# Performance work log

Measured on AMD Instinct MI355X. Metric: run time of the kernel, lower is better.

## Reference

```python
import jax, jax.numpy as jnp
import numpy as np

B, S, I, W, H = 32, 2048, 32, 20, 128  # batch, seq_len, input_size, window_size, hidden_size
LN_EPS = 1e-5


def setup_inputs() -> dict:
    key = jax.random.key(0)
    ks = jax.random.split(key, 12)
    sc = lambda fan: 1.0 / np.sqrt(fan)
    x = jax.random.normal(ks[0], (B, S, I), jnp.float32)
    # encoder: Linear(W*I -> H) + LayerNorm(H) (+ GELU, dropout inactive at eval)
    W_enc = jax.random.normal(ks[1], (W * I, H), jnp.float32) * sc(W * I)
    b_enc = jnp.zeros((H,), jnp.float32)
    gamma = jnp.ones((H,), jnp.float32)
    beta = jnp.zeros((H,), jnp.float32)
    # comparator: Linear(2H->H), GELU, Linear(H->H//2), GELU, Linear(H//2->1), Sigmoid
    W1 = jax.random.normal(ks[2], (2 * H, H), jnp.float32) * sc(2 * H)
    b1 = jnp.zeros((H,), jnp.float32)
    W2 = jax.random.normal(ks[3], (H, H // 2), jnp.float32) * sc(H)
    b2 = jnp.zeros((H // 2,), jnp.float32)
    W3 = jax.random.normal(ks[4], (H // 2, 1), jnp.float32) * sc(H // 2)
    b3 = jnp.zeros((1,), jnp.float32)
    return dict(x=x, W_enc=W_enc, b_enc=b_enc, gamma=gamma, beta=beta,
                W1=W1, b1=b1, W2=W2, b2=b2, W3=W3, b3=b3)


def _gelu(v):
    return jax.nn.gelu(v, approximate=False)  # torch nn.GELU default is exact erf


def reference(x, W_enc, b_enc, gamma, beta, W1, b1, W2, b2, W3, b3):
    Bs, Ss, Is = x.shape
    Wd = W_enc.shape[0] // Is  # window_size
    nwin = Ss - Wd + 1
    # gather all sliding windows once: (B, nwin, Wd*I)
    idx = jnp.arange(nwin)[:, None] + jnp.arange(Wd)[None, :]
    win = x[:, idx, :].reshape(Bs, nwin, Wd * Is)
    # encoder: one big GEMM over all windows (before(t) == window at t-Wd, after(t) == window at t)
    h = win @ W_enc + b_enc
    mu = jnp.mean(h, axis=-1, keepdims=True)
    var = jnp.mean((h - mu) ** 2, axis=-1, keepdims=True)
    enc = _gelu((h - mu) / jnp.sqrt(var + LN_EPS) * gamma + beta)  # (B, nwin, H)
    T = Ss - 2 * Wd  # number of valid changepoint positions t in [Wd, Ss-Wd)
    combined = jnp.concatenate([enc[:, :T], enc[:, Wd:Wd + T]], axis=-1)  # (B, T, 2H)
    z = _gelu(combined @ W1 + b1)
    z = _gelu(z @ W2 + b2)
    p = jax.nn.sigmoid((z @ W3 + b3)[..., 0])  # (B, T)
    probs = jnp.pad(p, ((0, 0), (Wd, Wd)))  # zero pad to (B, S)
    return probs, probs > 0.5
```

## Files before the change

### kernel.cpp

```cpp
#include <hip/hip_runtime.h>
#include <hip/hip_bf16.h>
#include <math.h>

namespace {

constexpr int kB = 32;
constexpr int kS = 2048;
constexpr int kI = 32;
constexpr int kW = 20;
constexpr int kH = 128;
constexpr int kNwin = kS - kW + 1;
constexpr int kT = kS - 2 * kW;
constexpr float kEps = 1e-5f;
constexpr int FCAP = 4096;
constexpr float kMargin = 1e-3f;

typedef __attribute__((ext_vector_type(8))) short short8;
typedef __attribute__((ext_vector_type(8))) unsigned short ush8;
typedef __attribute__((ext_vector_type(4))) float f32x4;

__device__ __forceinline__ unsigned short f2bf(float f) {
    unsigned u = __builtin_bit_cast(unsigned, f);
    u += 0x7FFFu + ((u >> 16) & 1u);
    return (unsigned short)(u >> 16);
}
__device__ __forceinline__ float bf2f(unsigned short h) {
    unsigned u = ((unsigned)h) << 16;
    return __builtin_bit_cast(float, u);
}
__device__ __forceinline__ void split2(float v, unsigned short& hi, unsigned short& lo) {
    hi = f2bf(v);
    lo = f2bf(v - bf2f(hi));
}
__device__ __forceinline__ float gelu_exact(float v) {
    return 0.5f * v * (1.0f + erff(v * 0.70710678118654752440f));
}

constexpr size_t ENCP_OFF = 0;
constexpr size_t WETH_OFF = 33554432;
constexpr size_t WETL_OFF = WETH_OFF + 163840;
constexpr size_t W1TH_OFF = WETL_OFF + 163840;
constexpr size_t W1TL_OFF = W1TH_OFF + 65536;
constexpr size_t W2TH_OFF = W1TL_OFF + 65536;
constexpr size_t W2TL_OFF = W2TH_OFF + 16384;
constexpr size_t FC_OFF   = W2TL_OFF + 16384;
constexpr size_t FL_OFF   = FC_OFF + 64;

__global__ void prep_kernel(const float* __restrict__ Wenc, const float* __restrict__ W1,
                            const float* __restrict__ W2,
                            unsigned short* __restrict__ WeTh, unsigned short* __restrict__ WeTl,
                            unsigned short* __restrict__ W1Th, unsigned short* __restrict__ W1Tl,
                            unsigned short* __restrict__ W2Th, unsigned short* __restrict__ W2Tl)
{
    const int tid = blockIdx.x * blockDim.x + threadIdx.x;
    const int nth = gridDim.x * blockDim.x;
    for (int i = tid; i < kH * 640; i += nth) {
        int n = i / 640, k = i - n * 640;
        split2(Wenc[(size_t)k * kH + n], WeTh[i], WeTl[i]);
    }
    for (int i = tid; i < kH * 256; i += nth) {
        int n = i >> 8, k = i & 255;
        split2(W1[(size_t)k * kH + n], W1Th[i], W1Tl[i]);
    }
    for (int i = tid; i < 64 * kH; i += nth) {
        int n = i >> 7, k = i & 127;
        split2(W2[(size_t)k * 64 + n], W2Th[i], W2Tl[i]);
    }
}

constexpr int AP = 40;

__global__ __launch_bounds__(256, 2)
void enc_kernel(const float* __restrict__ x,
                const unsigned short* __restrict__ WeTh, const unsigned short* __restrict__ WeTl,
                const float* __restrict__ benc, const float* __restrict__ gma,
                const float* __restrict__ bta, unsigned* __restrict__ encp)
{
    __shared__ unsigned short xsh[148 * AP];
    __shared__ unsigned short xsl[148 * AP];
    __shared__ unsigned short wth[128 * AP];
    __shared__ unsigned short wtl[128 * AP];
    __shared__ float prm[384];

    const int tid = threadIdx.x, b = blockIdx.y, t0 = blockIdx.x * 128;
    const int l = tid & 63, w = tid >> 6;
    const int cb = l & 15, rg = l >> 4;

    if (tid < 128) { prm[tid] = benc[tid]; prm[128 + tid] = gma[tid]; prm[256 + tid] = bta[tid]; }

    const float4* x4 = reinterpret_cast<const float4*>(x + (size_t)b * kS * kI);
    for (int i = tid; i < 148 * 8; i += 256) {
        int r = i >> 3, q = i & 7;
        int gr = t0 + r; if (gr > kS - 1) gr = kS - 1;
        float4 v = x4[gr * 8 + q];
        unsigned short h0, h1, h2, h3, l0, l1, l2, l3;
        split2(v.x, h0, l0); split2(v.y, h1, l1); split2(v.z, h2, l2); split2(v.w, h3, l3);
        *reinterpret_cast<uint2*>(&xsh[r * AP + q * 4]) =
            make_uint2((unsigned)h0 | ((unsigned)h1 << 16), (unsigned)h2 | ((unsigned)h3 << 16));
        *reinterpret_cast<uint2*>(&xsl[r * AP + q * 4]) =
            make_uint2((unsigned)l0 | ((unsigned)l1 << 16), (unsigned)l2 | ((unsigned)l3 << 16));
    }

    f32x4 acc[2][8];
    #pragma unroll
    for (int mi = 0; mi < 2; ++mi)
        #pragma unroll
        for (int nf = 0; nf < 8; ++nf) acc[mi][nf] = f32x4{0.f, 0.f, 0.f, 0.f};

    for (int kc = 0; kc < 20; ++kc) {
        __syncthreads();
        #pragma unroll
        for (int u = 0; u < 2; ++u) {
            int i = tid + 256 * u;
            int n = i >> 2, q = i & 3;
            *reinterpret_cast<ush8*>(&wth[n * AP + q * 8]) =
                *reinterpret_cast<const ush8*>(WeTh + (size_t)n * 640 + kc * 32 + q * 8);
            *reinterpret_cast<ush8*>(&wtl[n * AP + q * 8]) =
                *reinterpret_cast<const ush8*>(WeTl + (size_t)n * 640 + kc * 32 + q * 8);
        }
        __syncthreads();
        const int a0o = (w * 32 + cb + kc) * AP + rg * 8;
        const int a1o = a0o + 16 * AP;
        short8 a0h = *reinterpret_cast<const short8*>(&xsh[a0o]);
        short8 a0l = *reinterpret_cast<const short8*>(&xsl[a0o]);
        short8 a1h = *reinterpret_cast<const short8*>(&xsh[a1o]);
        short8 a1l = *reinterpret_cast<const short8*>(&xsl[a1o]);
        #pragma unroll
        for (int nf = 0; nf < 8; ++nf) {
            const int bo = (nf * 16 + cb) * AP + rg * 8;
            short8 bh = *reinterpret_cast<const short8*>(&wth[bo]);
            short8 bl = *reinterpret_cast<const short8*>(&wtl[bo]);
            acc[0][nf] = __builtin_amdgcn_mfma_f32_16x16x32_bf16(a0h, bh, acc[0][nf], 0, 0, 0);
            acc[0][nf] = __builtin_amdgcn_mfma_f32_16x16x32_bf16(a0l, bh, acc[0][nf], 0, 0, 0);
            acc[0][nf] = __builtin_amdgcn_mfma_f32_16x16x32_bf16(a0h, bl, acc[0][nf], 0, 0, 0);
            acc[1][nf] = __builtin_amdgcn_mfma_f32_16x16x32_bf16(a1h, bh, acc[1][nf], 0, 0, 0);
            acc[1][nf] = __builtin_amdgcn_mfma_f32_16x16x32_bf16(a1l, bh, acc[1][nf], 0, 0, 0);
            acc[1][nf] = __builtin_amdgcn_mfma_f32_16x16x32_bf16(a1h, bl, acc[1][nf], 0, 0, 0);
        }
    }

    #pragma unroll
    for (int mi = 0; mi < 2; ++mi) {
        #pragma unroll
        for (int r = 0; r < 4; ++r) {
            const int rl = w * 32 + mi * 16 + rg * 4 + r;
            const int t = t0 + rl;
            float h[8];
            float s = 0.f;
            #pragma unroll
            for (int nf = 0; nf < 8; ++nf) { h[nf] = acc[mi][nf][r] + prm[nf * 16 + cb]; s += h[nf]; }
            s += __shfl_xor(s, 1); s += __shfl_xor(s, 2); s += __shfl_xor(s, 4); s += __shfl_xor(s, 8);
            const float mu = s * (1.f / 128.f);
            float s2 = 0.f;
            #pragma unroll
            for (int nf = 0; nf < 8; ++nf) { h[nf] -= mu; s2 += h[nf] * h[nf]; }
            s2 += __shfl_xor(s2, 1); s2 += __shfl_xor(s2, 2); s2 += __shfl_xor(s2, 4); s2 += __shfl_xor(s2, 8);
            const float rstd = 1.f / sqrtf(s2 * (1.f / 128.f) + kEps);
            if (t < kNwin) {
                unsigned* dst = encp + ((size_t)(b * kS + t)) * kH;
                #pragma unroll
                for (int nf = 0; nf < 8; ++nf) {
                    float v = gelu_exact(h[nf] * rstd * prm[128 + nf * 16 + cb] + prm[256 + nf * 16 + cb]);
                    unsigned short hi, lo;
                    split2(v, hi, lo);
                    dst[nf * 16 + cb] = (unsigned)hi | ((unsigned)lo << 16);
                }
            }
        }
    }
}

__global__ __launch_bounds__(256, 2)
void cmp_kernel(const unsigned* __restrict__ encp,
                const unsigned short* __restrict__ W1Th, const unsigned short* __restrict__ W1Tl,
                const float* __restrict__ b1,
                const unsigned short* __restrict__ W2Th, const unsigned short* __restrict__ W2Tl,
                const float* __restrict__ b2, const float* __restrict__ W3,
                const float* __restrict__ b3, float* __restrict__ out,
                int* __restrict__ fcnt, unsigned* __restrict__ flist)
{
    __shared__ __align__(16) unsigned short pool[27648];
    __shared__ float prm[192];

    unsigned short* esh = pool;
    unsigned short* esl = pool + 2560;
    unsigned short* z1h = pool;
    unsigned short* z1l = pool + 8704;
    unsigned short* wth = pool + 17408;
    unsigned short* wtl = pool + 22528;
    float* z2f = reinterpret_cast<float*>(pool);

    const int tid = threadIdx.x, b = blockIdx.y, t0 = blockIdx.x * 64;
    const int l = tid & 63, w = tid >> 6;
    const int cb = l & 15, rg = l >> 4;

    if (tid < 128) prm[tid] = b1[tid];
    else if (tid < 192) prm[tid] = b2[tid - 128];

    f32x4 acc1[8];
    #pragma unroll
    for (int nf = 0; nf < 8; ++nf) acc1[nf] = f32x4{0.f, 0.f, 0.f, 0.f};

    for (int kc = 0; kc < 8; ++kc) {
        __syncthreads();
        const int ro = (kc < 4) ? 0 : kW, co = (kc & 3) * 32;
        {
            const int r = tid >> 2, q = tid & 3;
            int gr = t0 + ro + r; if (gr > kNwin - 1) gr = kNwin - 1;
            const unsigned* src = encp + ((size_t)(b * kS + gr)) * kH + co + q * 8;
            const uint4 v0 = *reinterpret_cast<const uint4*>(src);
            const uint4 v1 = *reinterpret_cast<const uint4*>(src + 4);
            *reinterpret_cast<uint2*>(&esh[r * AP + q * 8]) =
                make_uint2((v0.x & 0xFFFFu) | ((v0.y & 0xFFFFu) << 16),
                           (v0.z & 0xFFFFu) | ((v0.w & 0xFFFFu) << 16));
            *reinterpret_cast<uint2*>(&esh[r * AP + q * 8 + 4]) =
                make_uint2((v1.x & 0xFFFFu) | ((v1.y & 0xFFFFu) << 16),
                           (v1.z & 0xFFFFu) | ((v1.w & 0xFFFFu) << 16));
            *reinterpret_cast<uint2*>(&esl[r * AP + q * 8]) =
                make_uint2((v0.x >> 16) | (v0.y & 0xFFFF0000u),
                           (v0.z >> 16) | (v0.w & 0xFFFF0000u));
            *reinterpret_cast<uint2*>(&esl[r * AP + q * 8 + 4]) =
                make_uint2((v1.x >> 16) | (v1.y & 0xFFFF0000u),
                           (v1.z >> 16) | (v1.w & 0xFFFF0000u));
        }
        #pragma unroll
        for (int u = 0; u < 2; ++u) {
            int i = tid + 256 * u;
            int n = i >> 2, q = i & 3;
            *reinterpret_cast<ush8*>(&wth[n * AP + q * 8]) =
                *reinterpret_cast<const ush8*>(W1Th + (size_t)n * 256 + kc * 32 + q * 8);
            *reinterpret_cast<ush8*>(&wtl[n * AP + q * 8]) =
                *reinterpret_cast<const ush8*>(W1Tl + (size_t)n * 256 + kc * 32 + q * 8);
        }
        __syncthreads();
        const int ao = (w * 16 + cb) * AP + rg * 8;
        short8 ah = *reinterpret_cast<const short8*>(&esh[ao]);
        short8 al = *reinterpret_cast<const short8*>(&esl[ao]);
        #pragma unroll
        for (int nf = 0; nf < 8; ++nf) {
            const int bo = (nf * 16 + cb) * AP + rg * 8;
            short8 bh = *reinterpret_cast<const short8*>(&wth[bo]);
            short8 bl = *reinterpret_cast<const short8*>(&wtl[bo]);
            acc1[nf] = __builtin_amdgcn_mfma_f32_16x16x32_bf16(ah, bh, acc1[nf], 0, 0, 0);
            acc1[nf] = __builtin_amdgcn_mfma_f32_16x16x32_bf16(al, bh, acc1[nf], 0, 0, 0);
            acc1[nf] = __builtin_amdgcn_mfma_f32_16x16x32_bf16(ah, bl, acc1[nf], 0, 0, 0);
        }
    }
    __syncthreads();
    #pragma unroll
    for (int r = 0; r < 4; ++r) {
        const int row = w * 16 + rg * 4 + r;
        #pragma unroll
        for (int nf = 0; nf < 8; ++nf) {
            float v = gelu_exact(acc1[nf][r] + prm[nf * 16 + cb]);
            unsigned short hi, lo;
            split2(v, hi, lo);
            z1h[row * 136 + nf * 16 + cb] = hi;
            z1l[row * 136 + nf * 16 + cb] = lo;
        }
    }

    f32x4 acc2[4];
    #pragma unroll
    for (int nf = 0; nf < 4; ++nf) acc2[nf] = f32x4{0.f, 0.f, 0.f, 0.f};

    for (int kc = 0; kc < 4; ++kc) {
        __syncthreads();
        {
            int n = tid >> 2, q = tid & 3;
            *reinterpret_cast<ush8*>(&wth[n * AP + q * 8]) =
                *reinterpret_cast<const ush8*>(W2Th + (size_t)n * 128 + kc * 32 + q * 8);
            *reinterpret_cast<ush8*>(&wtl[n * AP + q * 8]) =
                *reinterpret_cast<const ush8*>(W2Tl + (size_t)n * 128 + kc * 32 + q * 8);
        }
        __syncthreads();
        const int ao = (w * 16 + cb) * 136 + kc * 32 + rg * 8;
        short8 ah = *reinterpret_cast<const short8*>(&z1h[ao]);
        short8 al = *reinterpret_cast<const short8*>(&z1l[ao]);
        #pragma unroll
        for (int nf = 0; nf < 4; ++nf) {
            const int bo = (nf * 16 + cb) * AP + rg * 8;
            short8 bh = *reinterpret_cast<const short8*>(&wth[bo]);
            short8 bl = *reinterpret_cast<const short8*>(&wtl[bo]);
            acc2[nf] = __builtin_amdgcn_mfma_f32_16x16x32_bf16(ah, bh, acc2[nf], 0, 0, 0);
            acc2[nf] = __builtin_amdgcn_mfma_f32_16x16x32_bf16(al, bh, acc2[nf], 0, 0, 0);
            acc2[nf] = __builtin_amdgcn_mfma_f32_16x16x32_bf16(ah, bl, acc2[nf], 0, 0, 0);
        }
    }
    __syncthreads();
    #pragma unroll
    for (int r = 0; r < 4; ++r) {
        const int row = w * 16 + rg * 4 + r;
        #pragma unroll
        for (int nf = 0; nf < 4; ++nf)
            z2f[row * 68 + nf * 16 + cb] = gelu_exact(acc2[nf][r] + prm[128 + nf * 16 + cb]);
    }
    __syncthreads();

    if (tid < 64) {
        const int t = t0 + tid;
        if (t < kT) {
            float s = 0.f;
            #pragma unroll 8
            for (int k = 0; k < 64; ++k) s = fmaf(z2f[tid * 68 + k], W3[k], s);
            const float p = 1.f / (1.f + expf(-(s + b3[0])));
            out[(size_t)b * kS + t + kW] = p;
            out[(size_t)kB * kS + (size_t)b * kS + t + kW] = (p > 0.5f) ? 1.f : 0.f;
            if (fabsf(p - 0.5f) < kMargin) {
                int idx = atomicAdd(fcnt, 1);
                if (idx < FCAP) flist[idx] = ((unsigned)b << 16) | (unsigned)t;
            }
        }
    }
}

__global__ __launch_bounds__(256, 4)
void fix2_kernel(const float* __restrict__ x, const float* __restrict__ Wenc,
                 const float* __restrict__ benc, const float* __restrict__ gma,
                 const float* __restrict__ bta, const float* __restrict__ W1,
                 const float* __restrict__ b1, const float* __restrict__ W2,
                 const float* __restrict__ b2, const float* __restrict__ W3,
                 const float* __restrict__ b3, const int* __restrict__ fcnt,
                 const unsigned* __restrict__ flist, float* __restrict__ out)
{
    __shared__ float xw[1280];
    __shared__ float es[256];
    __shared__ float z1s[128];
    __shared__ float z2s[64];
    __shared__ float wred[4];

    const int tid = threadIdx.x;
    int n = *fcnt; if (n > FCAP) n = FCAP;

    for (int i = blockIdx.x; i < n; i += gridDim.x) {
        const unsigned e = flist[i];
        const int b = (int)(e >> 16), t = (int)(e & 0xFFFF);
        __syncthreads();
        for (int j = tid; j < 320; j += 256) {
            int r = (j >= 160) ? 1 : 0, u = j - r * 160;
            const float4 v = *reinterpret_cast<const float4*>(
                x + ((size_t)b * kS + t + r * kW) * kI + u * 4);
            *reinterpret_cast<float4*>(&xw[r * 640 + u * 4]) = v;
        }
        __syncthreads();
        const int r = tid >> 7, c = tid & 127;
        float h = 0.f;
        const float* xr = &xw[r * 640];
        #pragma unroll 16
        for (int k = 0; k < 640; ++k) h = fmaf(xr[k], Wenc[(size_t)k * kH + c], h);
        h += benc[c];
        float s = h;
        #pragma unroll
        for (int m = 1; m < 64; m <<= 1) s += __shfl_xor(s, m, 64);
        if ((tid & 63) == 0) wred[tid >> 6] = s;
        __syncthreads();
        const float mu = (wred[r * 2] + wred[r * 2 + 1]) * (1.f / 128.f);
        const float d = h - mu;
        float s2 = d * d;
        #pragma unroll
        for (int m = 1; m < 64; m <<= 1) s2 += __shfl_xor(s2, m, 64);
        __syncthreads();
        if ((tid & 63) == 0) wred[tid >> 6] = s2;
        __syncthreads();
        const float var = (wred[r * 2] + wred[r * 2 + 1]) * (1.f / 128.f);
        es[tid] = gelu_exact(d * (1.f / sqrtf(var + kEps)) * gma[c] + bta[c]);
        __syncthreads();
        if (tid < kH) {
            float z = 0.f;
            #pragma unroll 16
            for (int k = 0; k < 256; ++k) z = fmaf(es[k], W1[(size_t)k * kH + tid], z);
            z1s[tid] = gelu_exact(z + b1[tid]);
        }
        __syncthreads();
        if (tid < 64) {
            float z = 0.f;
            #pragma unroll 16
            for (int k = 0; k < kH; ++k) z = fmaf(z1s[k], W2[(size_t)k * 64 + tid], z);
            z2s[tid] = gelu_exact(z + b2[tid]);
        }
        __syncthreads();
        if (tid < 64) {
            float s3 = z2s[tid] * W3[tid];
            #pragma unroll
            for (int m = 1; m < 64; m <<= 1) s3 += __shfl_xor(s3, m, 64);
            if (tid == 0) {
                const float p = 1.f / (1.f + expf(-(s3 + b3[0])));
                out[(size_t)b * kS + t + kW] = p;
                out[(size_t)kB * kS + (size_t)b * kS + t + kW] = (p > 0.5f) ? 1.f : 0.f;
            }
        }
        __syncthreads();
    }
}

}

extern "C" void kernel_launch(void* const* d_in, const int* in_sizes, int n_in,
                              void* d_out, int out_size, void* d_ws, size_t ws_size,
                              hipStream_t stream)
{
    const float* x    = (const float*)d_in[0];
    const float* Wenc = (const float*)d_in[1];
    const float* benc = (const float*)d_in[2];
    const float* gma  = (const float*)d_in[3];
    const float* bta  = (const float*)d_in[4];
    const float* W1   = (const float*)d_in[5];
    const float* b1   = (const float*)d_in[6];
    const float* W2   = (const float*)d_in[7];
    const float* b2   = (const float*)d_in[8];
    const float* W3   = (const float*)d_in[9];
    const float* b3   = (const float*)d_in[10];
    float* out = (float*)d_out;

    char* ws = (char*)d_ws;
    unsigned* encp        = (unsigned*)(ws + ENCP_OFF);
    unsigned short* WeTh  = (unsigned short*)(ws + WETH_OFF);
    unsigned short* WeTl  = (unsigned short*)(ws + WETL_OFF);
    unsigned short* W1Th  = (unsigned short*)(ws + W1TH_OFF);
    unsigned short* W1Tl  = (unsigned short*)(ws + W1TL_OFF);
    unsigned short* W2Th  = (unsigned short*)(ws + W2TH_OFF);
    unsigned short* W2Tl  = (unsigned short*)(ws + W2TL_OFF);
    int* fcnt             = (int*)(ws + FC_OFF);
    unsigned* flist       = (unsigned*)(ws + FL_OFF);

    hipMemsetAsync(d_out, 0, (size_t)out_size * sizeof(float), stream);
    hipMemsetAsync(fcnt, 0, 64, stream);

    prep_kernel<<<256, 256, 0, stream>>>(Wenc, W1, W2, WeTh, WeTl, W1Th, W1Tl, W2Th, W2Tl);
    enc_kernel<<<dim3(16, kB), 256, 0, stream>>>(x, WeTh, WeTl, benc, gma, bta, encp);
    cmp_kernel<<<dim3(32, kB), 256, 0, stream>>>(encp, W1Th, W1Tl, b1, W2Th, W2Tl, b2,
                                                 W3, b3, out, fcnt, flist);
    fix2_kernel<<<4096, 256, 0, stream>>>(x, Wenc, benc, gma, bta, W1, b1, W2, b2, W3, b3,
                                          fcnt, flist, out);
}
```

Before: 137.6 us.

## Double-buffer weight and activation tiles with register prefetch and swizzled LDS layout

The encoder and comparator GEMM loops now prefetch the next K-chunk of weights (and encoder activations) into registers while the MFMAs on the current chunk run, then write them to the other half of a double-buffered LDS area. This drops one barrier per iteration and hides global load latency behind compute. Weight tiles also move from a padded row stride to an XOR-swizzled 32-element layout to avoid LDS bank conflicts without padding. The cost is more registers held for the prefetch and a larger shared pool in the encoder, which could lower occupancy under the 2-blocks launch bound.

```diff
diff --git a/kernel.cpp b/kernel.cpp
--- a/kernel.cpp
+++ b/kernel.cpp
@@ -34,6 +34,9 @@
 }
 __device__ __forceinline__ float gelu_exact(float v) {
     return 0.5f * v * (1.0f + erff(v * 0.70710678118654752440f));
+}
+__device__ __forceinline__ int wsw(int n, int q) {
+    return n * 32 + ((q ^ ((n >> 1) & 3)) << 3);
 }
 
 constexpr size_t ENCP_OFF = 0;
@@ -76,11 +79,11 @@
                 const float* __restrict__ benc, const float* __restrict__ gma,
                 const float* __restrict__ bta, unsigned* __restrict__ encp)
 {
-    __shared__ unsigned short xsh[148 * AP];
-    __shared__ unsigned short xsl[148 * AP];
-    __shared__ unsigned short wth[128 * AP];
-    __shared__ unsigned short wtl[128 * AP];
+    __shared__ __align__(16) unsigned short pool[28144];
     __shared__ float prm[384];
+
+    unsigned short* xsh = pool;
+    unsigned short* xsl = pool + 5880;
 
     const int tid = threadIdx.x, b = blockIdx.y, t0 = blockIdx.x * 128;
     const int l = tid & 63, w = tid >> 6;
@@ -89,7 +92,7 @@
     if (tid < 128) { prm[tid] = benc[tid]; prm[128 + tid] = gma[tid]; prm[256 + tid] = bta[tid]; }
 
     const float4* x4 = reinterpret_cast<const float4*>(x + (size_t)b * kS * kI);
-    for (int i = tid; i < 148 * 8; i += 256) {
+    for (int i = tid; i < 147 * 8; i += 256) {
         int r = i >> 3, q = i & 7;
         int gr = t0 + r; if (gr > kS - 1) gr = kS - 1;
         float4 v = x4[gr * 8 + q];
@@ -101,35 +104,49 @@
             make_uint2((unsigned)l0 | ((unsigned)l1 << 16), (unsigned)l2 | ((unsigned)l3 << 16));
     }
 
+    const int n0 = tid >> 2, q0 = tid & 3;
+    const int wd0 = wsw(n0, q0), wd1 = wsw(n0 + 64, q0);
+    ush8 pwh0, pwl0, pwh1, pwl1;
+#define ELOADW(kc) { \
+    const unsigned short* sh = WeTh + (size_t)n0 * 640 + (kc) * 32 + q0 * 8; \
+    const unsigned short* sl = WeTl + (size_t)n0 * 640 + (kc) * 32 + q0 * 8; \
+    pwh0 = *reinterpret_cast<const ush8*>(sh); \
+    pwl0 = *reinterpret_cast<const ush8*>(sl); \
+    pwh1 = *reinterpret_cast<const ush8*>(sh + 64 * 640); \
+    pwl1 = *reinterpret_cast<const ush8*>(sl + 64 * 640); }
+#define EWRITEW(buf) { \
+    unsigned short* WH = pool + 11760 + (buf) * 8192; \
+    unsigned short* WL = WH + 4096; \
+    *reinterpret_cast<ush8*>(&WH[wd0]) = pwh0; \
+    *reinterpret_cast<ush8*>(&WH[wd1]) = pwh1; \
+    *reinterpret_cast<ush8*>(&WL[wd0]) = pwl0; \
+    *reinterpret_cast<ush8*>(&WL[wd1]) = pwl1; }
+
+    ELOADW(0); EWRITEW(0);
+    __syncthreads();
+
     f32x4 acc[2][8];
     #pragma unroll
     for (int mi = 0; mi < 2; ++mi)
         #pragma unroll
         for (int nf = 0; nf < 8; ++nf) acc[mi][nf] = f32x4{0.f, 0.f, 0.f, 0.f};
 
+    const int wb_r = cb * 32 + ((rg ^ ((cb >> 1) & 3)) << 3);
+
     for (int kc = 0; kc < 20; ++kc) {
-        __syncthreads();
-        #pragma unroll
-        for (int u = 0; u < 2; ++u) {
-            int i = tid + 256 * u;
-            int n = i >> 2, q = i & 3;
-            *reinterpret_cast<ush8*>(&wth[n * AP + q * 8]) =
-                *reinterpret_cast<const ush8*>(WeTh + (size_t)n * 640 + kc * 32 + q * 8);
-            *reinterpret_cast<ush8*>(&wtl[n * AP + q * 8]) =
-                *reinterpret_cast<const ush8*>(WeTl + (size_t)n * 640 + kc * 32 + q * 8);
-        }
-        __syncthreads();
+        const int cur = kc & 1;
+        if (kc < 19) ELOADW(kc + 1);
+        const unsigned short* WH = pool + 11760 + cur * 8192;
+        const unsigned short* WL = WH + 4096;
         const int a0o = (w * 32 + cb + kc) * AP + rg * 8;
-        const int a1o = a0o + 16 * AP;
         short8 a0h = *reinterpret_cast<const short8*>(&xsh[a0o]);
         short8 a0l = *reinterpret_cast<const short8*>(&xsl[a0o]);
-        short8 a1h = *reinterpret_cast<const short8*>(&xsh[a1o]);
-        short8 a1l = *reinterpret_cast<const short8*>(&xsl[a1o]);
+        short8 a1h = *reinterpret_cast<const short8*>(&xsh[a0o + 16 * AP]);
+        short8 a1l = *reinterpret_cast<const short8*>(&xsl[a0o + 16 * AP]);
         #pragma unroll
         for (int nf = 0; nf < 8; ++nf) {
-            const int bo = (nf * 16 + cb) * AP + rg * 8;
-            short8 bh = *reinterpret_cast<const short8*>(&wth[bo]);
-            short8 bl = *reinterpret_cast<const short8*>(&wtl[bo]);
+            short8 bh = *reinterpret_cast<const short8*>(&WH[nf * 512 + wb_r]);
+            short8 bl = *reinterpret_cast<const short8*>(&WL[nf * 512 + wb_r]);
             acc[0][nf] = __builtin_amdgcn_mfma_f32_16x16x32_bf16(a0h, bh, acc[0][nf], 0, 0, 0);
             acc[0][nf] = __builtin_amdgcn_mfma_f32_16x16x32_bf16(a0l, bh, acc[0][nf], 0, 0, 0);
             acc[0][nf] = __builtin_amdgcn_mfma_f32_16x16x32_bf16(a0h, bl, acc[0][nf], 0, 0, 0);
@@ -137,7 +154,11 @@
             acc[1][nf] = __builtin_amdgcn_mfma_f32_16x16x32_bf16(a1l, bh, acc[1][nf], 0, 0, 0);
             acc[1][nf] = __builtin_amdgcn_mfma_f32_16x16x32_bf16(a1h, bl, acc[1][nf], 0, 0, 0);
         }
-    }
+        if (kc < 19) EWRITEW(cur ^ 1);
+        __syncthreads();
+    }
+#undef ELOADW
+#undef EWRITEW
 
     #pragma unroll
     for (int mi = 0; mi < 2; ++mi) {
@@ -179,16 +200,8 @@
                 const float* __restrict__ b3, float* __restrict__ out,
                 int* __restrict__ fcnt, unsigned* __restrict__ flist)
 {
-    __shared__ __align__(16) unsigned short pool[27648];
+    __shared__ __align__(16) unsigned short pool[26624];
     __shared__ float prm[192];
-
-    unsigned short* esh = pool;
-    unsigned short* esl = pool + 2560;
-    unsigned short* z1h = pool;
-    unsigned short* z1l = pool + 8704;
-    unsigned short* wth = pool + 17408;
-    unsigned short* wtl = pool + 22528;
-    float* z2f = reinterpret_cast<float*>(pool);
 
     const int tid = threadIdx.x, b = blockIdx.y, t0 = blockIdx.x * 64;
     const int l = tid & 63, w = tid >> 6;
@@ -197,56 +210,95 @@
     if (tid < 128) prm[tid] = b1[tid];
     else if (tid < 192) prm[tid] = b2[tid - 128];
 
+    const int er = tid >> 2, eq = tid & 3;
+    const int n0 = tid >> 2, q0 = tid & 3;
+    const int wd0 = wsw(n0, q0), wd1 = wsw(n0 + 64, q0);
+    const int wb_r = cb * 32 + ((rg ^ ((cb >> 1) & 3)) << 3);
+
+    uint4 pe0, pe1;
+    ush8 p1h0, p1l0, p1h1, p1l1;
+#define CLOADES(kc) { \
+    const int ro = ((kc) < 4) ? 0 : kW, co = ((kc) & 3) * 32; \
+    int gr = t0 + ro + er; if (gr > kNwin - 1) gr = kNwin - 1; \
+    const unsigned* src = encp + ((size_t)(b * kS + gr)) * kH + co + eq * 8; \
+    pe0 = *reinterpret_cast<const uint4*>(src); \
+    pe1 = *reinterpret_cast<const uint4*>(src + 4); }
+#define CWRITEES(buf) { \
+    unsigned short* EH = pool + (buf) * 5120; \
+    unsigned short* EL = EH + 2560; \
+    *reinterpret_cast<uint2*>(&EH[er * AP + eq * 8]) = \
+        make_uint2((pe0.x & 0xFFFFu) | ((pe0.y & 0xFFFFu) << 16), \
+                   (pe0.z & 0xFFFFu) | ((pe0.w & 0xFFFFu) << 16)); \
+    *reinterpret_cast<uint2*>(&EH[er * AP + eq * 8 + 4]) = \
+        make_uint2((pe1.x & 0xFFFFu) | ((pe1.y & 0xFFFFu) << 16), \
+                   (pe1.z & 0xFFFFu) | ((pe1.w & 0xFFFFu) << 16)); \
+    *reinterpret_cast<uint2*>(&EL[er * AP + eq * 8]) = \
+        make_uint2((pe0.x >> 16) | (pe0.y & 0xFFFF0000u), \
+                   (pe0.z >> 16) | (pe0.w & 0xFFFF0000u)); \
+    *reinterpret_cast<uint2*>(&EL[er * AP + eq * 8 + 4]) = \
+        make_uint2((pe1.x >> 16) | (pe1.y & 0xFFFF0000u), \
+                   (pe1.z >> 16) | (pe1.w & 0xFFFF0000u)); }
+#define CLOADW1(kc) { \
+    const unsigned short* sh = W1Th + (size_t)n0 * 256 + (kc) * 32 + q0 * 8; \
+    const unsigned short* sl = W1Tl + (size_t)n0 * 256 + (kc) * 32 + q0 * 8; \
+    p1h0 = *reinterpret_cast<const ush8*>(sh); \
+    p1l0 = *reinterpret_cast<const ush8*>(sl); \
+    p1h1 = *reinterpret_cast<const ush8*>(sh + 64 * 256); \
+    p1l1 = *reinterpret_cast<const ush8*>(sl + 64 * 256); }
+#define CWRITEW1(buf) { \
+    unsigned short* WH = pool + 10240 + (buf) * 8192; \
+    unsigned short* WL = WH + 4096; \
+    *reinterpret_cast<ush8*>(&WH[wd0]) = p1h0; \
+    *reinterpret_cast<ush8*>(&WH[wd1]) = p1h1; \
+    *reinterpret_cast<ush8*>(&WL[wd0]) = p1l0; \
+    *reinterpret_cast<ush8*>(&WL[wd1]) = p1l1; }
+
+    CLOADES(0); CLOADW1(0); CWRITEES(0); CWRITEW1(0);
+    __syncthreads();
+
     f32x4 acc1[8];
     #pragma unroll
     for (int nf = 0; nf < 8; ++nf) acc1[nf] = f32x4{0.f, 0.f, 0.f, 0.f};
 
     for (int kc = 0; kc < 8; ++kc) {
-        __syncthreads();
-        const int ro = (kc < 4) ? 0 : kW, co = (kc & 3) * 32;
-        {
-            const int r = tid >> 2, q = tid & 3;
-            int gr = t0 + ro + r; if (gr > kNwin - 1) gr = kNwin - 1;
-            const unsigned* src = encp + ((size_t)(b * kS + gr)) * kH + co + q * 8;
-            const uint4 v0 = *reinterpret_cast<const uint4*>(src);
-            const uint4 v1 = *reinterpret_cast<const uint4*>(src + 4);
-            *reinterpret_cast<uint2*>(&esh[r * AP + q * 8]) =
-                make_uint2((v0.x & 0xFFFFu) | ((v0.y & 0xFFFFu) << 16),
-                           (v0.z & 0xFFFFu) | ((v0.w & 0xFFFFu) << 16));
-            *reinterpret_cast<uint2*>(&esh[r * AP + q * 8 + 4]) =
-                make_uint2((v1.x & 0xFFFFu) | ((v1.y & 0xFFFFu) << 16),
-                           (v1.z & 0xFFFFu) | ((v1.w & 0xFFFFu) << 16));
-            *reinterpret_cast<uint2*>(&esl[r * AP + q * 8]) =
-                make_uint2((v0.x >> 16) | (v0.y & 0xFFFF0000u),
-                           (v0.z >> 16) | (v0.w & 0xFFFF0000u));
-            *reinterpret_cast<uint2*>(&esl[r * AP + q * 8 + 4]) =
-                make_uint2((v1.x >> 16) | (v1.y & 0xFFFF0000u),
-                           (v1.z >> 16) | (v1.w & 0xFFFF0000u));
-        }
-        #pragma unroll
-        for (int u = 0; u < 2; ++u) {
-            int i = tid + 256 * u;
-            int n = i >> 2, q = i & 3;
-            *reinterpret_cast<ush8*>(&wth[n * AP + q * 8]) =
-                *reinterpret_cast<const ush8*>(W1Th + (size_t)n * 256 + kc * 32 + q * 8);
-            *reinterpret_cast<ush8*>(&wtl[n * AP + q * 8]) =
-                *reinterpret_cast<const ush8*>(W1Tl + (size_t)n * 256 + kc * 32 + q * 8);
-        }
-        __syncthreads();
+        const int cur = kc & 1;
+        if (kc < 7) { CLOADES(kc + 1); CLOADW1(kc + 1); }
+        const unsigned short* EH = pool + cur * 5120;
+        const unsigned short* EL = EH + 2560;
+        const unsigned short* WH = pool + 10240 + cur * 8192;
+        const unsigned short* WL = WH + 4096;
         const int ao = (w * 16 + cb) * AP + rg * 8;
-        short8 ah = *reinterpret_cast<const short8*>(&esh[ao]);
-        short8 al = *reinterpret_cast<const short8*>(&esl[ao]);
+        short8 ah = *reinterpret_cast<const short8*>(&EH[ao]);
+        short8 al = *reinterpret_cast<const short8*>(&EL[ao]);
         #pragma unroll
         for (int nf = 0; nf < 8; ++nf) {
-            const int bo = (nf * 16 + cb) * AP + rg * 8;
-            short8 bh = *reinterpret_cast<const short8*>(&wth[bo]);
-            short8 bl = *reinterpret_cast<const short8*>(&wtl[bo]);
+            short8 bh = *reinterpret_cast<const short8*>(&WH[nf * 512 + wb_r]);
+            short8 bl = *reinterpret_cast<const short8*>(&WL[nf * 512 + wb_r]);
             acc1[nf] = __builtin_amdgcn_mfma_f32_16x16x32_bf16(ah, bh, acc1[nf], 0, 0, 0);
             acc1[nf] = __builtin_amdgcn_mfma_f32_16x16x32_bf16(al, bh, acc1[nf], 0, 0, 0);
             acc1[nf] = __builtin_amdgcn_mfma_f32_16x16x32_bf16(ah, bl, acc1[nf], 0, 0, 0);
         }
-    }
-    __syncthreads();
+        if (kc < 7) { CWRITEES(cur ^ 1); CWRITEW1(cur ^ 1); }
+        __syncthreads();
+    }
+#undef CLOADES
+#undef CWRITEES
+#undef CLOADW1
+#undef CWRITEW1
+
+    unsigned short* z1h = pool;
+    unsigned short* z1l = pool + 8704;
+    ush8 p2h, p2l;
+#define CLOADW2(kc) { \
+    p2h = *reinterpret_cast<const ush8*>(W2Th + (size_t)n0 * 128 + (kc) * 32 + q0 * 8); \
+    p2l = *reinterpret_cast<const ush8*>(W2Tl + (size_t)n0 * 128 + (kc) * 32 + q0 * 8); }
+#define CWRITEW2(buf) { \
+    unsigned short* WH = pool + 17408 + (buf) * 4096; \
+    unsigned short* WL = WH + 2048; \
+    *reinterpret_cast<ush8*>(&WH[wd0]) = p2h; \
+    *reinterpret_cast<ush8*>(&WL[wd0]) = p2l; }
+
+    CLOADW2(0);
     #pragma unroll
     for (int r = 0; r < 4; ++r) {
         const int row = w * 16 + rg * 4 + r;
@@ -259,35 +311,36 @@
             z1l[row * 136 + nf * 16 + cb] = lo;
         }
     }
+    CWRITEW2(0);
+    __syncthreads();
 
     f32x4 acc2[4];
     #pragma unroll
     for (int nf = 0; nf < 4; ++nf) acc2[nf] = f32x4{0.f, 0.f, 0.f, 0.f};
 
     for (int kc = 0; kc < 4; ++kc) {
-        __syncthreads();
-        {
-            int n = tid >> 2, q = tid & 3;
-            *reinterpret_cast<ush8*>(&wth[n * AP + q * 8]) =
-                *reinterpret_cast<const ush8*>(W2Th + (size_t)n * 128 + kc * 32 + q * 8);
-            *reinterpret_cast<ush8*>(&wtl[n * AP + q * 8]) =
-                *reinterpret_cast<const ush8*>(W2Tl + (size_t)n * 128 + kc * 32 + q * 8);
-        }
-        __syncthreads();
+        const int cur = kc & 1;
+        if (kc < 3) CLOADW2(kc + 1);
+        const unsigned short* WH = pool + 17408 + cur * 4096;
+        const unsigned short* WL = WH + 2048;
         const int ao = (w * 16 + cb) * 136 + kc * 32 + rg * 8;
         short8 ah = *reinterpret_cast<const short8*>(&z1h[ao]);
         short8 al = *reinterpret_cast<const short8*>(&z1l[ao]);
         #pragma unroll
         for (int nf = 0; nf < 4; ++nf) {
-            const int bo = (nf * 16 + cb) * AP + rg * 8;
-            short8 bh = *reinterpret_cast<const short8*>(&wth[bo]);
-            short8 bl = *reinterpret_cast<const short8*>(&wtl[bo]);
+            short8 bh = *reinterpret_cast<const short8*>(&WH[nf * 512 + wb_r]);
+            short8 bl = *reinterpret_cast<const short8*>(&WL[nf * 512 + wb_r]);
             acc2[nf] = __builtin_amdgcn_mfma_f32_16x16x32_bf16(ah, bh, acc2[nf], 0, 0, 0);
             acc2[nf] = __builtin_amdgcn_mfma_f32_16x16x32_bf16(al, bh, acc2[nf], 0, 0, 0);
             acc2[nf] = __builtin_amdgcn_mfma_f32_16x16x32_bf16(ah, bl, acc2[nf], 0, 0, 0);
         }
-    }
-    __syncthreads();
+        if (kc < 3) CWRITEW2(cur ^ 1);
+        __syncthreads();
+    }
+#undef CLOADW2
+#undef CWRITEW2
+
+    float* z2f = reinterpret_cast<float*>(pool);
     #pragma unroll
     for (int r = 0; r < 4; ++r) {
         const int row = w * 16 + rg * 4 + r;
```

Result: no change. 136.7 us (-0.6%).

## Enlarge encoder tile to 256 rows and stage cmp encodings once in LDS

Applied to the files above, without the earlier changes.

The encoder kernel now processes 256 windows per block with 512 threads, so each staged weight chunk serves twice as many rows and the x halo overhead is amortised. LN parameters move from shared memory into registers. The comparator kernel loads the full 84-row encoding slab into LDS once, up front, instead of re-reading global memory per K chunk, and unpacks the hi/lo bf16 halves at fragment-load time. Shared memory per cmp block rises to about 64KB, which may reduce occupancy.

```diff
diff --git a/kernel.cpp b/kernel.cpp
--- a/kernel.cpp
+++ b/kernel.cpp
@@ -69,27 +69,25 @@
 }
 
 constexpr int AP = 40;
-
-__global__ __launch_bounds__(256, 2)
+constexpr int EXR = 275;
+
+__global__ __launch_bounds__(512, 2)
 void enc_kernel(const float* __restrict__ x,
                 const unsigned short* __restrict__ WeTh, const unsigned short* __restrict__ WeTl,
                 const float* __restrict__ benc, const float* __restrict__ gma,
                 const float* __restrict__ bta, unsigned* __restrict__ encp)
 {
-    __shared__ unsigned short xsh[148 * AP];
-    __shared__ unsigned short xsl[148 * AP];
+    __shared__ unsigned short xsh[EXR * AP];
+    __shared__ unsigned short xsl[EXR * AP];
     __shared__ unsigned short wth[128 * AP];
     __shared__ unsigned short wtl[128 * AP];
-    __shared__ float prm[384];
-
-    const int tid = threadIdx.x, b = blockIdx.y, t0 = blockIdx.x * 128;
+
+    const int tid = threadIdx.x, b = blockIdx.y, t0 = blockIdx.x * 256;
     const int l = tid & 63, w = tid >> 6;
     const int cb = l & 15, rg = l >> 4;
 
-    if (tid < 128) { prm[tid] = benc[tid]; prm[128 + tid] = gma[tid]; prm[256 + tid] = bta[tid]; }
-
     const float4* x4 = reinterpret_cast<const float4*>(x + (size_t)b * kS * kI);
-    for (int i = tid; i < 148 * 8; i += 256) {
+    for (int i = tid; i < EXR * 8; i += 512) {
         int r = i >> 3, q = i & 7;
         int gr = t0 + r; if (gr > kS - 1) gr = kS - 1;
         float4 v = x4[gr * 8 + q];
@@ -109,22 +107,20 @@
 
     for (int kc = 0; kc < 20; ++kc) {
         __syncthreads();
-        #pragma unroll
-        for (int u = 0; u < 2; ++u) {
-            int i = tid + 256 * u;
-            int n = i >> 2, q = i & 3;
+        {
+            const int n = tid >> 2, q = tid & 3;
+            const size_t so = (size_t)n * 640 + kc * 32 + q * 8;
             *reinterpret_cast<ush8*>(&wth[n * AP + q * 8]) =
-                *reinterpret_cast<const ush8*>(WeTh + (size_t)n * 640 + kc * 32 + q * 8);
+                *reinterpret_cast<const ush8*>(WeTh + so);
             *reinterpret_cast<ush8*>(&wtl[n * AP + q * 8]) =
-                *reinterpret_cast<const ush8*>(WeTl + (size_t)n * 640 + kc * 32 + q * 8);
+                *reinterpret_cast<const ush8*>(WeTl + so);
         }
         __syncthreads();
         const int a0o = (w * 32 + cb + kc) * AP + rg * 8;
-        const int a1o = a0o + 16 * AP;
         short8 a0h = *reinterpret_cast<const short8*>(&xsh[a0o]);
         short8 a0l = *reinterpret_cast<const short8*>(&xsl[a0o]);
-        short8 a1h = *reinterpret_cast<const short8*>(&xsh[a1o]);
-        short8 a1l = *reinterpret_cast<const short8*>(&xsl[a1o]);
+        short8 a1h = *reinterpret_cast<const short8*>(&xsh[a0o + 16 * AP]);
+        short8 a1l = *reinterpret_cast<const short8*>(&xsl[a0o + 16 * AP]);
         #pragma unroll
         for (int nf = 0; nf < 8; ++nf) {
             const int bo = (nf * 16 + cb) * AP + rg * 8;
@@ -139,6 +135,13 @@
         }
     }
 
+    float bv[8], gv[8], btv[8];
+    #pragma unroll
+    for (int nf = 0; nf < 8; ++nf) {
+        bv[nf]  = benc[nf * 16 + cb];
+        gv[nf]  = gma[nf * 16 + cb];
+        btv[nf] = bta[nf * 16 + cb];
+    }
     #pragma unroll
     for (int mi = 0; mi < 2; ++mi) {
         #pragma unroll
@@ -148,7 +151,7 @@
             float h[8];
             float s = 0.f;
             #pragma unroll
-            for (int nf = 0; nf < 8; ++nf) { h[nf] = acc[mi][nf][r] + prm[nf * 16 + cb]; s += h[nf]; }
+            for (int nf = 0; nf < 8; ++nf) { h[nf] = acc[mi][nf][r] + bv[nf]; s += h[nf]; }
             s += __shfl_xor(s, 1); s += __shfl_xor(s, 2); s += __shfl_xor(s, 4); s += __shfl_xor(s, 8);
             const float mu = s * (1.f / 128.f);
             float s2 = 0.f;
@@ -160,7 +163,7 @@
                 unsigned* dst = encp + ((size_t)(b * kS + t)) * kH;
                 #pragma unroll
                 for (int nf = 0; nf < 8; ++nf) {
-                    float v = gelu_exact(h[nf] * rstd * prm[128 + nf * 16 + cb] + prm[256 + nf * 16 + cb]);
+                    float v = gelu_exact(h[nf] * rstd * gv[nf] + btv[nf]);
                     unsigned short hi, lo;
                     split2(v, hi, lo);
                     dst[nf * 16 + cb] = (unsigned)hi | ((unsigned)lo << 16);
@@ -169,6 +172,8 @@
         }
     }
 }
+
+constexpr int ESP = 132;
 
 __global__ __launch_bounds__(256, 2)
 void cmp_kernel(const unsigned* __restrict__ encp,
@@ -179,23 +184,23 @@
                 const float* __restrict__ b3, float* __restrict__ out,
                 int* __restrict__ fcnt, unsigned* __restrict__ flist)
 {
-    __shared__ __align__(16) unsigned short pool[27648];
-    __shared__ float prm[192];
-
-    unsigned short* esh = pool;
-    unsigned short* esl = pool + 2560;
-    unsigned short* z1h = pool;
-    unsigned short* z1l = pool + 8704;
-    unsigned short* wth = pool + 17408;
-    unsigned short* wtl = pool + 22528;
-    float* z2f = reinterpret_cast<float*>(pool);
+    __shared__ __align__(16) unsigned char poolb[64832];
+
+    unsigned* es         = reinterpret_cast<unsigned*>(poolb);
+    unsigned short* wt1h = reinterpret_cast<unsigned short*>(poolb + 44352);
+    unsigned short* wt1l = reinterpret_cast<unsigned short*>(poolb + 54592);
 
     const int tid = threadIdx.x, b = blockIdx.y, t0 = blockIdx.x * 64;
     const int l = tid & 63, w = tid >> 6;
     const int cb = l & 15, rg = l >> 4;
 
-    if (tid < 128) prm[tid] = b1[tid];
-    else if (tid < 192) prm[tid] = b2[tid - 128];
+    for (int i = tid; i < 84 * 32; i += 256) {
+        int r = i >> 5, u = i & 31;
+        int gr = t0 + r; if (gr > kNwin - 1) gr = kNwin - 1;
+        const uint4 v = *reinterpret_cast<const uint4*>(
+            encp + ((size_t)(b * kS + gr)) * kH + u * 4);
+        *reinterpret_cast<uint4*>(&es[r * ESP + u * 4]) = v;
+    }
 
     f32x4 acc1[8];
     #pragma unroll
@@ -203,56 +208,50 @@
 
     for (int kc = 0; kc < 8; ++kc) {
         __syncthreads();
-        const int ro = (kc < 4) ? 0 : kW, co = (kc & 3) * 32;
-        {
-            const int r = tid >> 2, q = tid & 3;
-            int gr = t0 + ro + r; if (gr > kNwin - 1) gr = kNwin - 1;
-            const unsigned* src = encp + ((size_t)(b * kS + gr)) * kH + co + q * 8;
-            const uint4 v0 = *reinterpret_cast<const uint4*>(src);
-            const uint4 v1 = *reinterpret_cast<const uint4*>(src + 4);
-            *reinterpret_cast<uint2*>(&esh[r * AP + q * 8]) =
-                make_uint2((v0.x & 0xFFFFu) | ((v0.y & 0xFFFFu) << 16),
-                           (v0.z & 0xFFFFu) | ((v0.w & 0xFFFFu) << 16));
-            *reinterpret_cast<uint2*>(&esh[r * AP + q * 8 + 4]) =
-                make_uint2((v1.x & 0xFFFFu) | ((v1.y & 0xFFFFu) << 16),
-                           (v1.z & 0xFFFFu) | ((v1.w & 0xFFFFu) << 16));
-            *reinterpret_cast<uint2*>(&esl[r * AP + q * 8]) =
-                make_uint2((v0.x >> 16) | (v0.y & 0xFFFF0000u),
-                           (v0.z >> 16) | (v0.w & 0xFFFF0000u));
-            *reinterpret_cast<uint2*>(&esl[r * AP + q * 8 + 4]) =
-                make_uint2((v1.x >> 16) | (v1.y & 0xFFFF0000u),
-                           (v1.z >> 16) | (v1.w & 0xFFFF0000u));
-        }
         #pragma unroll
         for (int u = 0; u < 2; ++u) {
             int i = tid + 256 * u;
             int n = i >> 2, q = i & 3;
-            *reinterpret_cast<ush8*>(&wth[n * AP + q * 8]) =
-                *reinterpret_cast<const ush8*>(W1Th + (size_t)n * 256 + kc * 32 + q * 8);
-            *reinterpret_cast<ush8*>(&wtl[n * AP + q * 8]) =
-                *reinterpret_cast<const ush8*>(W1Tl + (size_t)n * 256 + kc * 32 + q * 8);
-        }
-        __syncthreads();
-        const int ao = (w * 16 + cb) * AP + rg * 8;
-        short8 ah = *reinterpret_cast<const short8*>(&esh[ao]);
-        short8 al = *reinterpret_cast<const short8*>(&esl[ao]);
+            const size_t so = (size_t)n * 256 + kc * 32 + q * 8;
+            *reinterpret_cast<ush8*>(&wt1h[n * AP + q * 8]) =
+                *reinterpret_cast<const ush8*>(W1Th + so);
+            *reinterpret_cast<ush8*>(&wt1l[n * AP + q * 8]) =
+                *reinterpret_cast<const ush8*>(W1Tl + so);
+        }
+        __syncthreads();
+        const int ro = (kc < 4) ? 0 : kW, co = (kc & 3) * 32;
+        const unsigned* ep = es + (w * 16 + cb + ro) * ESP + co + rg * 8;
+        const uint4 v0 = *reinterpret_cast<const uint4*>(ep);
+        const uint4 v1 = *reinterpret_cast<const uint4*>(ep + 4);
+        const uint4 ahw = make_uint4(
+            (v0.x & 0xFFFFu) | ((v0.y & 0xFFFFu) << 16), (v0.z & 0xFFFFu) | ((v0.w & 0xFFFFu) << 16),
+            (v1.x & 0xFFFFu) | ((v1.y & 0xFFFFu) << 16), (v1.z & 0xFFFFu) | ((v1.w & 0xFFFFu) << 16));
+        const uint4 alw = make_uint4(
+            (v0.x >> 16) | (v0.y & 0xFFFF0000u), (v0.z >> 16) | (v0.w & 0xFFFF0000u),
+            (v1.x >> 16) | (v1.y & 0xFFFF0000u), (v1.z >> 16) | (v1.w & 0xFFFF0000u));
+        short8 ah = __builtin_bit_cast(short8, ahw);
+        short8 al = __builtin_bit_cast(short8, alw);
         #pragma unroll
         for (int nf = 0; nf < 8; ++nf) {
             const int bo = (nf * 16 + cb) * AP + rg * 8;
-            short8 bh = *reinterpret_cast<const short8*>(&wth[bo]);
-            short8 bl = *reinterpret_cast<const short8*>(&wtl[bo]);
+            short8 bh = *reinterpret_cast<const short8*>(&wt1h[bo]);
+            short8 bl = *reinterpret_cast<const short8*>(&wt1l[bo]);
             acc1[nf] = __builtin_amdgcn_mfma_f32_16x16x32_bf16(ah, bh, acc1[nf], 0, 0, 0);
             acc1[nf] = __builtin_amdgcn_mfma_f32_16x16x32_bf16(al, bh, acc1[nf], 0, 0, 0);
             acc1[nf] = __builtin_amdgcn_mfma_f32_16x16x32_bf16(ah, bl, acc1[nf], 0, 0, 0);
         }
     }
     __syncthreads();
+    unsigned short* z1h = reinterpret_cast<unsigned short*>(poolb);
+    unsigned short* z1l = reinterpret_cast<unsigned short*>(poolb + 17408);
+    unsigned short* w2h = reinterpret_cast<unsigned short*>(poolb + 34816);
+    unsigned short* w2l = reinterpret_cast<unsigned short*>(poolb + 39936);
     #pragma unroll
     for (int r = 0; r < 4; ++r) {
         const int row = w * 16 + rg * 4 + r;
         #pragma unroll
         for (int nf = 0; nf < 8; ++nf) {
-            float v = gelu_exact(acc1[nf][r] + prm[nf * 16 + cb]);
+            float v = gelu_exact(acc1[nf][r] + b1[nf * 16 + cb]);
             unsigned short hi, lo;
             split2(v, hi, lo);
             z1h[row * 136 + nf * 16 + cb] = hi;
@@ -267,11 +266,12 @@
     for (int kc = 0; kc < 4; ++kc) {
         __syncthreads();
         {
-            int n = tid >> 2, q = tid & 3;
-            *reinterpret_cast<ush8*>(&wth[n * AP + q * 8]) =
-                *reinterpret_cast<const ush8*>(W2Th + (size_t)n * 128 + kc * 32 + q * 8);
-            *reinterpret_cast<ush8*>(&wtl[n * AP + q * 8]) =
-                *reinterpret_cast<const ush8*>(W2Tl + (size_t)n * 128 + kc * 32 + q * 8);
+            const int n = tid >> 2, q = tid & 3;
+            const size_t so = (size_t)n * 128 + kc * 32 + q * 8;
+            *reinterpret_cast<ush8*>(&w2h[n * AP + q * 8]) =
+                *reinterpret_cast<const ush8*>(W2Th + so);
+            *reinterpret_cast<ush8*>(&w2l[n * AP + q * 8]) =
+                *reinterpret_cast<const ush8*>(W2Tl + so);
         }
         __syncthreads();
         const int ao = (w * 16 + cb) * 136 + kc * 32 + rg * 8;
@@ -280,20 +280,21 @@
         #pragma unroll
         for (int nf = 0; nf < 4; ++nf) {
             const int bo = (nf * 16 + cb) * AP + rg * 8;
-            short8 bh = *reinterpret_cast<const short8*>(&wth[bo]);
-            short8 bl = *reinterpret_cast<const short8*>(&wtl[bo]);
+            short8 bh = *reinterpret_cast<const short8*>(&w2h[bo]);
+            short8 bl = *reinterpret_cast<const short8*>(&w2l[bo]);
             acc2[nf] = __builtin_amdgcn_mfma_f32_16x16x32_bf16(ah, bh, acc2[nf], 0, 0, 0);
             acc2[nf] = __builtin_amdgcn_mfma_f32_16x16x32_bf16(al, bh, acc2[nf], 0, 0, 0);
             acc2[nf] = __builtin_amdgcn_mfma_f32_16x16x32_bf16(ah, bl, acc2[nf], 0, 0, 0);
         }
     }
     __syncthreads();
+    float* z2f = reinterpret_cast<float*>(poolb);
     #pragma unroll
     for (int r = 0; r < 4; ++r) {
         const int row = w * 16 + rg * 4 + r;
         #pragma unroll
         for (int nf = 0; nf < 4; ++nf)
-            z2f[row * 68 + nf * 16 + cb] = gelu_exact(acc2[nf][r] + prm[128 + nf * 16 + cb]);
+            z2f[row * 68 + nf * 16 + cb] = gelu_exact(acc2[nf][r] + b2[nf * 16 + cb]);
     }
     __syncthreads();
 
@@ -427,7 +428,7 @@
     hipMemsetAsync(fcnt, 0, 64, stream);
 
     prep_kernel<<<256, 256, 0, stream>>>(Wenc, W1, W2, WeTh, WeTl, W1Th, W1Tl, W2Th, W2Tl);
-    enc_kernel<<<dim3(16, kB), 256, 0, stream>>>(x, WeTh, WeTl, benc, gma, bta, encp);
+    enc_kernel<<<dim3(8, kB), 512, 0, stream>>>(x, WeTh, WeTl, benc, gma, bta, encp);
     cmp_kernel<<<dim3(32, kB), 256, 0, stream>>>(encp, W1Th, W1Tl, b1, W2Th, W2Tl, b2,
                                                  W3, b3, out, fcnt, flist);
     fix2_kernel<<<4096, 256, 0, stream>>>(x, Wenc, benc, gma, bta, W1, b1, W2, b2, W3, b3,
```

Result: slower. 144.6 us (+5.1%).
